# Kernel tuning notes

Hardware: AMD Instinct MI355X
Metric: run time of the kernel (lower is better)

The kernel has to match this reference:

```python
import jax, jax.numpy as jnp
import numpy as np

FP16_MIN = -65504.0
FP16_MAX = 65504.0

B, S, D, H = 2, 2048, 1024, 16
HD = D // H


def setup_inputs() -> dict:
    key = jax.random.key(0)
    ks = jax.random.split(key, 12)
    s = 0.02
    inp = {
        "x_q": jax.random.normal(ks[0], (B, S, D), jnp.float32),
        "x_k": jax.random.normal(ks[1], (B, S, D), jnp.float32),
        "x_v": jax.random.normal(ks[2], (B, S, D), jnp.float32),
        # causal mask [B, 1, S, S]; 0 entries are masked out
        "mask": jnp.broadcast_to(jnp.tril(jnp.ones((S, S), jnp.int32)), (B, 1, S, S)),
        "Wq": jax.random.normal(ks[3], (D, D), jnp.float32) * s,
        "bq": jnp.zeros((D,), jnp.float32),
        "Wk": jax.random.normal(ks[4], (D, D), jnp.float32) * s,
        "bk": jnp.zeros((D,), jnp.float32),
        "Wv": jax.random.normal(ks[5], (D, D), jnp.float32) * s,
        "bv": jnp.zeros((D,), jnp.float32),
        "Wo": jax.random.normal(ks[6], (D, D), jnp.float32) * s,
        "bo": jnp.zeros((D,), jnp.float32),
    }
    return inp


def _split_heads(x):
    # [B, S, D] -> [B, H, S, HD]
    b, s, _ = x.shape
    return x.reshape(b, s, H, HD).transpose(0, 2, 1, 3)


def reference(x_q, x_k, x_v, mask, Wq, bq, Wk, bk, Wv, bv, Wo, bo):
    scale = jnp.sqrt(jnp.float32(HD))
    q = _split_heads(x_q @ Wq + bq)  # [B,H,S,HD]
    k = _split_heads(x_k @ Wk + bk)
    v = _split_heads(x_v @ Wv + bv)

    scores = jnp.einsum("bhqd,bhkd->bhqk", q, k) / scale  # [B,H,S,S]
    scores = jnp.where(mask == 0, FP16_MIN, scores)
    scores = jnp.where(jnp.isneginf(scores), FP16_MIN, scores)
    scores = jnp.where(jnp.isposinf(scores), FP16_MAX, scores)

    probs = jax.nn.softmax(scores, axis=-1)  # dropout p=0.0 -> identity
    ctx = jnp.einsum("bhqk,bhkd->bhqd", probs, v)  # [B,H,S,HD]
    ctx = ctx.transpose(0, 2, 1, 3).reshape(x_q.shape[0], x_q.shape[1], D)
    out = ctx @ Wo + bo
    return out, probs
```

## Files before the change

### kernel.cpp

```cpp
#include <hip/hip_runtime.h>


typedef __bf16 bf16x8 __attribute__((ext_vector_type(8)));
typedef float f32x4 __attribute__((ext_vector_type(4)));

__device__ __forceinline__ unsigned short f2bf(float f) {
  unsigned int u = __builtin_bit_cast(unsigned int, f);
  u += 0x7fffu + ((u >> 16) & 1u);
  return (unsigned short)(u >> 16);
}
__device__ __forceinline__ float bf2f_lo(unsigned int u) {
  return __builtin_bit_cast(float, u << 16);
}
__device__ __forceinline__ float bf2f_hi(unsigned int u) {
  return __builtin_bit_cast(float, u & 0xffff0000u);
}

__global__ void transpose_w(const float* __restrict__ W0, const float* __restrict__ W1,
                            const float* __restrict__ W2, const float* __restrict__ W3,
                            unsigned short* __restrict__ Wt) {
  __shared__ float t[32][33];
  const int z = blockIdx.z;
  const float* W = (z == 0) ? W0 : (z == 1) ? W1 : (z == 2) ? W2 : W3;
  unsigned short* o = Wt + (size_t)z * 1048576u;
  const int n0 = blockIdx.x * 32, k0 = blockIdx.y * 32;
  const int tx = threadIdx.x, ty = threadIdx.y;
#pragma unroll
  for (int i = 0; i < 4; i++)
    t[ty + 8 * i][tx] = W[(size_t)(k0 + ty + 8 * i) * 1024 + n0 + tx];
  __syncthreads();
#pragma unroll
  for (int i = 0; i < 4; i++)
    o[(size_t)(n0 + ty + 8 * i) * 1024 + k0 + tx] = f2bf(t[tx][ty + 8 * i]);
}

__global__ __launch_bounds__(256) void gemm_kernel(
    const void* __restrict__ A0, const void* __restrict__ A1, const void* __restrict__ A2,
    const unsigned short* __restrict__ Wtb,
    const float* __restrict__ b0, const float* __restrict__ b1, const float* __restrict__ b2,
    void* __restrict__ O0, void* __restrict__ O1, void* __restrict__ O2,
    const int mode0) {
  __shared__ unsigned short Alds[64 * 72];
  const int z = blockIdx.z;
  const int mode = mode0 + z;
  const void* Av = (z == 0) ? A0 : (z == 1) ? A1 : A2;
  const float* bias = (z == 0) ? b0 : (z == 1) ? b1 : b2;
  void* outv = (z == 0) ? O0 : (z == 1) ? O1 : O2;
  const unsigned short* Wt = Wtb + (size_t)z * 1048576u;

  const int tid = threadIdx.x;
  const int lane = tid & 63;
  const int wave = tid >> 6;
  const int wm = wave >> 1, wn = wave & 1;
  const int m0 = blockIdx.y * 64, n0 = blockIdx.x * 128;
  const int g = lane >> 4, c = lane & 15;

  f32x4 acc[2][4];
#pragma unroll
  for (int i = 0; i < 2; i++)
#pragma unroll
    for (int j = 0; j < 4; j++) acc[i][j] = (f32x4){0.f, 0.f, 0.f, 0.f};

  const int srow = tid >> 2;
  const int sch = (tid & 3) * 16;

  uint4 pk0, pk1;
#define LOAD_PACK(KB)                                                             \
  if (mode < 3) {                                                                 \
    const float* A = (const float*)Av;                                            \
    const float4* src = (const float4*)(A + (size_t)(m0 + srow) * 1024 + (KB) + sch); \
    const float4 v0 = src[0], v1 = src[1], v2 = src[2], v3 = src[3];              \
    pk0.x = (unsigned int)f2bf(v0.x) | ((unsigned int)f2bf(v0.y) << 16);          \
    pk0.y = (unsigned int)f2bf(v0.z) | ((unsigned int)f2bf(v0.w) << 16);          \
    pk0.z = (unsigned int)f2bf(v1.x) | ((unsigned int)f2bf(v1.y) << 16);          \
    pk0.w = (unsigned int)f2bf(v1.z) | ((unsigned int)f2bf(v1.w) << 16);          \
    pk1.x = (unsigned int)f2bf(v2.x) | ((unsigned int)f2bf(v2.y) << 16);          \
    pk1.y = (unsigned int)f2bf(v2.z) | ((unsigned int)f2bf(v2.w) << 16);          \
    pk1.z = (unsigned int)f2bf(v3.x) | ((unsigned int)f2bf(v3.y) << 16);          \
    pk1.w = (unsigned int)f2bf(v3.z) | ((unsigned int)f2bf(v3.w) << 16);          \
  } else {                                                                        \
    const unsigned short* A = (const unsigned short*)Av;                          \
    const uint4* src = (const uint4*)(A + (size_t)(m0 + srow) * 1024 + (KB) + sch); \
    pk0 = src[0];                                                                 \
    pk1 = src[1];                                                                 \
  }

  LOAD_PACK(0);
  for (int kb = 0; kb < 1024; kb += 64) {
    *(uint4*)&Alds[srow * 72 + sch] = pk0;
    *(uint4*)&Alds[srow * 72 + sch + 8] = pk1;
    if (kb + 64 < 1024) { LOAD_PACK(kb + 64); }
    __syncthreads();

    bf16x8 af[2][2], bfr[4][2];
#pragma unroll
    for (int mi = 0; mi < 2; mi++)
#pragma unroll
      for (int kk = 0; kk < 2; kk++)
        af[mi][kk] = *(const bf16x8*)&Alds[(wm * 32 + mi * 16 + c) * 72 + kk * 32 + g * 8];
#pragma unroll
    for (int nf = 0; nf < 4; nf++)
#pragma unroll
      for (int kk = 0; kk < 2; kk++)
        bfr[nf][kk] = *(const bf16x8*)(Wt + (size_t)(n0 + wn * 64 + nf * 16 + c) * 1024 + kb + kk * 32 + g * 8);
#pragma unroll
    for (int kk = 0; kk < 2; kk++)
#pragma unroll
      for (int mi = 0; mi < 2; mi++)
#pragma unroll
        for (int nf = 0; nf < 4; nf++)
          acc[mi][nf] = __builtin_amdgcn_mfma_f32_16x16x32_bf16(af[mi][kk], bfr[nf][kk], acc[mi][nf], 0, 0, 0);
    __syncthreads();
  }
#undef LOAD_PACK

#pragma unroll
  for (int nf = 0; nf < 4; nf++) {
    const int col = n0 + wn * 64 + nf * 16 + c;
    const float bc = bias[col];
#pragma unroll
    for (int mi = 0; mi < 2; mi++) {
#pragma unroll
      for (int r = 0; r < 4; r++) {
        const int row = m0 + wm * 32 + mi * 16 + g * 4 + r;
        const float v = acc[mi][nf][r] + bc;
        if (mode == 0) {
          ((unsigned short*)outv)[(size_t)row * 1024 + col] = f2bf(v * 0.125f);
        } else if (mode == 1) {
          ((unsigned short*)outv)[(size_t)row * 1024 + col] = f2bf(v);
        } else if (mode == 2) {
          const int bb = row >> 11, s = row & 2047;
          ((unsigned short*)outv)[((size_t)(bb * 1024 + col)) * 2048 + s] = f2bf(v);
        } else {
          ((float*)outv)[(size_t)row * 1024 + col] = v;
        }
      }
    }
  }
}

__global__ __launch_bounds__(512, 4) void attn_kernel(
    const unsigned short* __restrict__ Q, const unsigned short* __restrict__ K,
    const unsigned short* __restrict__ Vt, float* __restrict__ probs,
    unsigned short* __restrict__ ctx) {
  __shared__ unsigned short Klds[64 * 72];
  __shared__ unsigned short Vlds[64 * 72];
  __shared__ unsigned short Plds[128 * 72];

  const int tid = threadIdx.x;
  const int lane = tid & 63, wave = tid >> 6;
  const int g = lane >> 4, c = lane & 15;
  const int bh = blockIdx.x;
  const int b = bh >> 4, h = bh & 15;
  const int q0 = blockIdx.y * 128;
  const int qrow0 = q0 + wave * 16;
  const int wave_kend = qrow0 + 16;

  const unsigned short* Qh = Q + ((size_t)(b * 2048 + qrow0)) * 1024 + h * 64;
  const unsigned short* Kh = K + ((size_t)b * 2048) * 1024 + h * 64;
  const unsigned short* Vh = Vt + ((size_t)bh) * 64 * 2048;
  float* Ph = probs + ((size_t)(bh * 2048 + q0)) * 2048;

  const bf16x8 qa0 = *(const bf16x8*)&Qh[(size_t)c * 1024 + g * 8];
  const bf16x8 qa1 = *(const bf16x8*)&Qh[(size_t)c * 1024 + 32 + g * 8];

  const int srow = tid >> 3;
  const int scol = (tid & 7) * 8;
  const int kb_end = q0 + 128;

  float lp[4] = {0.f, 0.f, 0.f, 0.f};
  f32x4 cacc[4];
#pragma unroll
  for (int nf = 0; nf < 4; nf++) cacc[nf] = (f32x4){0.f, 0.f, 0.f, 0.f};

  uint4 kreg = *(const uint4*)(Kh + (size_t)srow * 1024 + scol);
  uint4 vreg = *(const uint4*)(Vh + (size_t)srow * 2048 + scol);
  for (int kb = 0; kb < kb_end; kb += 64) {
    *(uint4*)&Klds[srow * 72 + scol] = kreg;
    *(uint4*)&Vlds[srow * 72 + scol] = vreg;
    if (kb + 64 < kb_end) {
      kreg = *(const uint4*)(Kh + (size_t)(kb + 64 + srow) * 1024 + scol);
      vreg = *(const uint4*)(Vh + (size_t)srow * 2048 + kb + 64 + scol);
    }
    __syncthreads();

    if (kb < wave_kend) {
      f32x4 sv[4];
#pragma unroll
      for (int sub = 0; sub < 4; sub++) {
        sv[sub] = (f32x4){0.f, 0.f, 0.f, 0.f};
        const unsigned short* Kr = &Klds[(sub * 16 + c) * 72];
        sv[sub] = __builtin_amdgcn_mfma_f32_16x16x32_bf16(qa0, *(const bf16x8*)&Kr[g * 8], sv[sub], 0, 0, 0);
        sv[sub] = __builtin_amdgcn_mfma_f32_16x16x32_bf16(qa1, *(const bf16x8*)&Kr[32 + g * 8], sv[sub], 0, 0, 0);
      }
      if (kb + 63 > qrow0) {
#pragma unroll
        for (int sub = 0; sub < 4; sub++)
#pragma unroll
          for (int r = 0; r < 4; r++)
            if (kb + sub * 16 + c > qrow0 + g * 4 + r) sv[sub][r] = -1e30f;
      }
#pragma unroll
      for (int sub = 0; sub < 4; sub++)
#pragma unroll
        for (int r = 0; r < 4; r++) {
          const float pu = __expf(sv[sub][r]);
          lp[r] += pu;
          Plds[(wave * 16 + g * 4 + r) * 72 + sub * 16 + c] = f2bf(pu);
        }
      const bf16x8 pa0 = *(const bf16x8*)&Plds[(wave * 16 + c) * 72 + g * 8];
      const bf16x8 pa1 = *(const bf16x8*)&Plds[(wave * 16 + c) * 72 + 32 + g * 8];
#pragma unroll
      for (int nf = 0; nf < 4; nf++) {
        const bf16x8 vf0 = *(const bf16x8*)&Vlds[(nf * 16 + c) * 72 + g * 8];
        const bf16x8 vf1 = *(const bf16x8*)&Vlds[(nf * 16 + c) * 72 + 32 + g * 8];
        cacc[nf] = __builtin_amdgcn_mfma_f32_16x16x32_bf16(pa0, vf0, cacc[nf], 0, 0, 0);
        cacc[nf] = __builtin_amdgcn_mfma_f32_16x16x32_bf16(pa1, vf1, cacc[nf], 0, 0, 0);
      }
    }
    __syncthreads();

    {
      const int prow = tid >> 2;
      const int pcb = (tid & 3) * 16;
      unsigned short* dst = (unsigned short*)Ph + (size_t)prow * 4096 + kb + pcb;
      const int rw_kend = q0 + (prow & ~15) + 16;
      if (kb < rw_kend) {
        *(uint4*)dst = *(const uint4*)&Plds[prow * 72 + pcb];
        *(uint4*)(dst + 8) = *(const uint4*)&Plds[prow * 72 + pcb + 8];
      } else {
        *(uint4*)dst = make_uint4(0u, 0u, 0u, 0u);
        *(uint4*)(dst + 8) = make_uint4(0u, 0u, 0u, 0u);
      }
    }
  }

#pragma unroll
  for (int off = 1; off < 16; off <<= 1)
#pragma unroll
    for (int r = 0; r < 4; r++) lp[r] += __shfl_xor(lp[r], off);
  float invl[4];
#pragma unroll
  for (int r = 0; r < 4; r++) invl[r] = 1.0f / lp[r];

#pragma unroll
  for (int nf = 0; nf < 4; nf++)
#pragma unroll
    for (int r = 0; r < 4; r++)
      ctx[((size_t)(b * 2048 + qrow0 + g * 4 + r)) * 1024 + h * 64 + nf * 16 + c] =
          f2bf(cacc[nf][r] * invl[r]);
}

__global__ __launch_bounds__(256) void norm_probs(float* __restrict__ probs) {
  __shared__ float wsum[4];
  const int rowIdx = blockIdx.x;
  const int q = rowIdx & 2047;
  const int kbe = ((q >> 7) + 1) << 7;
  float* base = probs + (size_t)rowIdx * 2048;
  const int t = threadIdx.x;
  const int c0 = t * 8;

  uint4 raw = make_uint4(0u, 0u, 0u, 0u);
  if (c0 < kbe) raw = *(const uint4*)((const unsigned short*)base + c0);
  float f0 = bf2f_lo(raw.x), f1 = bf2f_hi(raw.x), f2 = bf2f_lo(raw.y), f3 = bf2f_hi(raw.y);
  float f4 = bf2f_lo(raw.z), f5 = bf2f_hi(raw.z), f6 = bf2f_lo(raw.w), f7 = bf2f_hi(raw.w);

  float s = ((f0 + f1) + (f2 + f3)) + ((f4 + f5) + (f6 + f7));
#pragma unroll
  for (int off = 1; off < 64; off <<= 1) s += __shfl_xor(s, off);
  if ((t & 63) == 0) wsum[t >> 6] = s;
  __syncthreads();
  const float il = 1.0f / (wsum[0] + wsum[1] + wsum[2] + wsum[3]);

  float4* dst = (float4*)(base + c0);
  dst[0] = make_float4(f0 * il, f1 * il, f2 * il, f3 * il);
  dst[1] = make_float4(f4 * il, f5 * il, f6 * il, f7 * il);
}

extern "C" void kernel_launch(void* const* d_in, const int* in_sizes, int n_in,
                              void* d_out, int out_size, void* d_ws, size_t ws_size,
                              hipStream_t stream) {
  if (ws_size < (size_t)40 * 1024 * 1024) return;

  const float* xq = (const float*)d_in[0];
  const float* xk = (const float*)d_in[1];
  const float* xv = (const float*)d_in[2];
  const float* Wq = (const float*)d_in[4];
  const float* bq = (const float*)d_in[5];
  const float* Wk = (const float*)d_in[6];
  const float* bk = (const float*)d_in[7];
  const float* Wv = (const float*)d_in[8];
  const float* bv = (const float*)d_in[9];
  const float* Wo = (const float*)d_in[10];
  const float* bo = (const float*)d_in[11];

  unsigned short* ws = (unsigned short*)d_ws;
  unsigned short* Wt = ws;
  unsigned short* Qw = ws + (size_t)4 * 1048576u;
  unsigned short* Kw = Qw + 4194304u;
  unsigned short* Vtw = Kw + 4194304u;
  unsigned short* Cw = Vtw + 4194304u;

  float* out = (float*)d_out;
  float* probs = out + 4194304u;

  transpose_w<<<dim3(32, 32, 4), dim3(32, 8), 0, stream>>>(Wq, Wk, Wv, Wo, Wt);
  gemm_kernel<<<dim3(8, 64, 3), 256, 0, stream>>>(xq, xk, xv, Wt, bq, bk, bv,
                                                  Qw, Kw, Vtw, 0);
  attn_kernel<<<dim3(32, 16, 1), 512, 0, stream>>>(Qw, Kw, Vtw, probs, Cw);
  norm_probs<<<dim3(65536), 256, 0, stream>>>(probs);
  gemm_kernel<<<dim3(8, 64, 1), 256, 0, stream>>>(Cw, Cw, Cw, Wt + 3u * 1048576u,
                                                  bo, bo, bo, out, out, out, 3);
}
```

Measured before the change: 363.7 us.

## Double-buffer K/V tiles, reverse block order, per-wave P writes, wave-per-row normalize

```diff
diff --git a/kernel.cpp b/kernel.cpp
--- a/kernel.cpp
+++ b/kernel.cpp
@@ -143,8 +143,8 @@
     const unsigned short* __restrict__ Q, const unsigned short* __restrict__ K,
     const unsigned short* __restrict__ Vt, float* __restrict__ probs,
     unsigned short* __restrict__ ctx) {
-  __shared__ unsigned short Klds[64 * 72];
-  __shared__ unsigned short Vlds[64 * 72];
+  __shared__ unsigned short Klds[2][64 * 72];
+  __shared__ unsigned short Vlds[2][64 * 72];
   __shared__ unsigned short Plds[128 * 72];
 
   const int tid = threadIdx.x;
@@ -152,7 +152,7 @@
   const int g = lane >> 4, c = lane & 15;
   const int bh = blockIdx.x;
   const int b = bh >> 4, h = bh & 15;
-  const int q0 = blockIdx.y * 128;
+  const int q0 = (int)(gridDim.y - 1 - blockIdx.y) * 128;
   const int qrow0 = q0 + wave * 16;
   const int wave_kend = qrow0 + 16;
 
@@ -173,23 +173,38 @@
 #pragma unroll
   for (int nf = 0; nf < 4; nf++) cacc[nf] = (f32x4){0.f, 0.f, 0.f, 0.f};
 
-  uint4 kreg = *(const uint4*)(Kh + (size_t)srow * 1024 + scol);
-  uint4 vreg = *(const uint4*)(Vh + (size_t)srow * 2048 + scol);
-  for (int kb = 0; kb < kb_end; kb += 64) {
-    *(uint4*)&Klds[srow * 72 + scol] = kreg;
-    *(uint4*)&Vlds[srow * 72 + scol] = vreg;
-    if (kb + 64 < kb_end) {
-      kreg = *(const uint4*)(Kh + (size_t)(kb + 64 + srow) * 1024 + scol);
-      vreg = *(const uint4*)(Vh + (size_t)srow * 2048 + kb + 64 + scol);
+  const int prow = lane >> 2;
+  const int pcb = (lane & 3) * 16;
+  unsigned short* PwOut = (unsigned short*)Ph + (size_t)(wave * 16 + prow) * 4096 + pcb;
+  const unsigned short* PwLds = &Plds[(wave * 16 + prow) * 72 + pcb];
+
+  {
+    const uint4 k0 = *(const uint4*)(Kh + (size_t)srow * 1024 + scol);
+    const uint4 v0 = *(const uint4*)(Vh + (size_t)srow * 2048 + scol);
+    *(uint4*)&Klds[0][srow * 72 + scol] = k0;
+    *(uint4*)&Vlds[0][srow * 72 + scol] = v0;
+  }
+
+  int cur = 0;
+  for (int kb = 0; kb < kb_end; kb += 64, cur ^= 1) {
+    uint4 kn, vn;
+    const bool more = (kb + 64) < kb_end;
+    if (more) {
+      kn = *(const uint4*)(Kh + (size_t)(kb + 64 + srow) * 1024 + scol);
+      vn = *(const uint4*)(Vh + (size_t)srow * 2048 + kb + 64 + scol);
     }
     __syncthreads();
+    if (more) {
+      *(uint4*)&Klds[cur ^ 1][srow * 72 + scol] = kn;
+      *(uint4*)&Vlds[cur ^ 1][srow * 72 + scol] = vn;
+    }
 
     if (kb < wave_kend) {
       f32x4 sv[4];
 #pragma unroll
       for (int sub = 0; sub < 4; sub++) {
         sv[sub] = (f32x4){0.f, 0.f, 0.f, 0.f};
-        const unsigned short* Kr = &Klds[(sub * 16 + c) * 72];
+        const unsigned short* Kr = &Klds[cur][(sub * 16 + c) * 72];
         sv[sub] = __builtin_amdgcn_mfma_f32_16x16x32_bf16(qa0, *(const bf16x8*)&Kr[g * 8], sv[sub], 0, 0, 0);
         sv[sub] = __builtin_amdgcn_mfma_f32_16x16x32_bf16(qa1, *(const bf16x8*)&Kr[32 + g * 8], sv[sub], 0, 0, 0);
       }
@@ -212,26 +227,18 @@
       const bf16x8 pa1 = *(const bf16x8*)&Plds[(wave * 16 + c) * 72 + 32 + g * 8];
 #pragma unroll
       for (int nf = 0; nf < 4; nf++) {
-        const bf16x8 vf0 = *(const bf16x8*)&Vlds[(nf * 16 + c) * 72 + g * 8];
-        const bf16x8 vf1 = *(const bf16x8*)&Vlds[(nf * 16 + c) * 72 + 32 + g * 8];
+        const bf16x8 vf0 = *(const bf16x8*)&Vlds[cur][(nf * 16 + c) * 72 + g * 8];
+        const bf16x8 vf1 = *(const bf16x8*)&Vlds[cur][(nf * 16 + c) * 72 + 32 + g * 8];
         cacc[nf] = __builtin_amdgcn_mfma_f32_16x16x32_bf16(pa0, vf0, cacc[nf], 0, 0, 0);
         cacc[nf] = __builtin_amdgcn_mfma_f32_16x16x32_bf16(pa1, vf1, cacc[nf], 0, 0, 0);
       }
-    }
-    __syncthreads();
-
-    {
-      const int prow = tid >> 2;
-      const int pcb = (tid & 3) * 16;
-      unsigned short* dst = (unsigned short*)Ph + (size_t)prow * 4096 + kb + pcb;
-      const int rw_kend = q0 + (prow & ~15) + 16;
-      if (kb < rw_kend) {
-        *(uint4*)dst = *(const uint4*)&Plds[prow * 72 + pcb];
-        *(uint4*)(dst + 8) = *(const uint4*)&Plds[prow * 72 + pcb + 8];
-      } else {
-        *(uint4*)dst = make_uint4(0u, 0u, 0u, 0u);
-        *(uint4*)(dst + 8) = make_uint4(0u, 0u, 0u, 0u);
-      }
+      unsigned short* dst = PwOut + kb;
+      *(uint4*)dst = *(const uint4*)PwLds;
+      *(uint4*)(dst + 8) = *(const uint4*)(PwLds + 8);
+    } else {
+      unsigned short* dst = PwOut + kb;
+      *(uint4*)dst = make_uint4(0u, 0u, 0u, 0u);
+      *(uint4*)(dst + 8) = make_uint4(0u, 0u, 0u, 0u);
     }
   }
 
@@ -252,29 +259,39 @@
 }
 
 __global__ __launch_bounds__(256) void norm_probs(float* __restrict__ probs) {
-  __shared__ float wsum[4];
-  const int rowIdx = blockIdx.x;
-  const int q = rowIdx & 2047;
-  const int kbe = ((q >> 7) + 1) << 7;
-  float* base = probs + (size_t)rowIdx * 2048;
-  const int t = threadIdx.x;
-  const int c0 = t * 8;
-
-  uint4 raw = make_uint4(0u, 0u, 0u, 0u);
-  if (c0 < kbe) raw = *(const uint4*)((const unsigned short*)base + c0);
-  float f0 = bf2f_lo(raw.x), f1 = bf2f_hi(raw.x), f2 = bf2f_lo(raw.y), f3 = bf2f_hi(raw.y);
-  float f4 = bf2f_lo(raw.z), f5 = bf2f_hi(raw.z), f6 = bf2f_lo(raw.w), f7 = bf2f_hi(raw.w);
-
-  float s = ((f0 + f1) + (f2 + f3)) + ((f4 + f5) + (f6 + f7));
-#pragma unroll
-  for (int off = 1; off < 64; off <<= 1) s += __shfl_xor(s, off);
-  if ((t & 63) == 0) wsum[t >> 6] = s;
-  __syncthreads();
-  const float il = 1.0f / (wsum[0] + wsum[1] + wsum[2] + wsum[3]);
-
-  float4* dst = (float4*)(base + c0);
-  dst[0] = make_float4(f0 * il, f1 * il, f2 * il, f3 * il);
-  dst[1] = make_float4(f4 * il, f5 * il, f6 * il, f7 * il);
+  const int wv = (blockIdx.x * 256 + threadIdx.x) >> 6;
+  const int lane = threadIdx.x & 63;
+  for (int row = wv; row < 65536; row += 8192) {
+    const int q = row & 2047;
+    const int kbe = ((q >> 7) + 1) << 7;
+    float* base = probs + (size_t)row * 2048;
+    const int c0 = lane * 32;
+    uint4 r0 = make_uint4(0u, 0u, 0u, 0u), r1 = r0, r2 = r0, r3 = r0;
+    if (c0 < kbe) {
+      const uint4* src = (const uint4*)((const unsigned short*)base + c0);
+      r0 = src[0]; r1 = src[1]; r2 = src[2]; r3 = src[3];
+    }
+    float f[32];
+#pragma unroll
+    for (int i = 0; i < 4; i++) {
+      const uint4 rr = (i == 0) ? r0 : (i == 1) ? r1 : (i == 2) ? r2 : r3;
+      f[i * 8 + 0] = bf2f_lo(rr.x); f[i * 8 + 1] = bf2f_hi(rr.x);
+      f[i * 8 + 2] = bf2f_lo(rr.y); f[i * 8 + 3] = bf2f_hi(rr.y);
+      f[i * 8 + 4] = bf2f_lo(rr.z); f[i * 8 + 5] = bf2f_hi(rr.z);
+      f[i * 8 + 6] = bf2f_lo(rr.w); f[i * 8 + 7] = bf2f_hi(rr.w);
+    }
+    float s = 0.f;
+#pragma unroll
+    for (int i = 0; i < 32; i++) s += f[i];
+#pragma unroll
+    for (int off = 1; off < 64; off <<= 1) s += __shfl_xor(s, off);
+    const float il = 1.0f / s;
+    float4* dst = (float4*)(base + c0);
+#pragma unroll
+    for (int i = 0; i < 8; i++)
+      dst[i] = make_float4(f[i * 4 + 0] * il, f[i * 4 + 1] * il,
+                           f[i * 4 + 2] * il, f[i * 4 + 3] * il);
+  }
 }
 
 extern "C" void kernel_launch(void* const* d_in, const int* in_sizes, int n_in,
@@ -308,7 +325,7 @@
   gemm_kernel<<<dim3(8, 64, 3), 256, 0, stream>>>(xq, xk, xv, Wt, bq, bk, bv,
                                                   Qw, Kw, Vtw, 0);
   attn_kernel<<<dim3(32, 16, 1), 512, 0, stream>>>(Qw, Kw, Vtw, probs, Cw);
-  norm_probs<<<dim3(65536), 256, 0, stream>>>(probs);
+  norm_probs<<<dim3(2048), 256, 0, stream>>>(probs);
   gemm_kernel<<<dim3(8, 64, 1), 256, 0, stream>>>(Cw, Cw, Cw, Wt + 3u * 1048576u,
                                                   bo, bo, bo, out, out, out, 3);
 }
```

Result: slower. 499.0 us (+37.2%).

## Double-buffer K/V in attention, fold log2e into Q scale, reverse block order

Applied to the files above, without the earlier changes.

```diff
diff --git a/kernel.cpp b/kernel.cpp
--- a/kernel.cpp
+++ b/kernel.cpp
@@ -8,6 +8,9 @@
   unsigned int u = __builtin_bit_cast(unsigned int, f);
   u += 0x7fffu + ((u >> 16) & 1u);
   return (unsigned short)(u >> 16);
+}
+__device__ __forceinline__ unsigned short f2bf_hw(float f) {
+  return __builtin_bit_cast(unsigned short, (__bf16)f);
 }
 __device__ __forceinline__ float bf2f_lo(unsigned int u) {
   return __builtin_bit_cast(float, u << 16);
@@ -125,7 +128,7 @@
         const int row = m0 + wm * 32 + mi * 16 + g * 4 + r;
         const float v = acc[mi][nf][r] + bc;
         if (mode == 0) {
-          ((unsigned short*)outv)[(size_t)row * 1024 + col] = f2bf(v * 0.125f);
+          ((unsigned short*)outv)[(size_t)row * 1024 + col] = f2bf(v * 0.1803368801111244f);
         } else if (mode == 1) {
           ((unsigned short*)outv)[(size_t)row * 1024 + col] = f2bf(v);
         } else if (mode == 2) {
@@ -143,8 +146,8 @@
     const unsigned short* __restrict__ Q, const unsigned short* __restrict__ K,
     const unsigned short* __restrict__ Vt, float* __restrict__ probs,
     unsigned short* __restrict__ ctx) {
-  __shared__ unsigned short Klds[64 * 72];
-  __shared__ unsigned short Vlds[64 * 72];
+  __shared__ unsigned short Klds[2][64 * 72];
+  __shared__ unsigned short Vlds[2][64 * 72];
   __shared__ unsigned short Plds[128 * 72];
 
   const int tid = threadIdx.x;
@@ -152,7 +155,7 @@
   const int g = lane >> 4, c = lane & 15;
   const int bh = blockIdx.x;
   const int b = bh >> 4, h = bh & 15;
-  const int q0 = blockIdx.y * 128;
+  const int q0 = (int)(gridDim.y - 1 - blockIdx.y) * 128;
   const int qrow0 = q0 + wave * 16;
   const int wave_kend = qrow0 + 16;
 
@@ -173,23 +176,36 @@
 #pragma unroll
   for (int nf = 0; nf < 4; nf++) cacc[nf] = (f32x4){0.f, 0.f, 0.f, 0.f};
 
-  uint4 kreg = *(const uint4*)(Kh + (size_t)srow * 1024 + scol);
-  uint4 vreg = *(const uint4*)(Vh + (size_t)srow * 2048 + scol);
-  for (int kb = 0; kb < kb_end; kb += 64) {
-    *(uint4*)&Klds[srow * 72 + scol] = kreg;
-    *(uint4*)&Vlds[srow * 72 + scol] = vreg;
-    if (kb + 64 < kb_end) {
-      kreg = *(const uint4*)(Kh + (size_t)(kb + 64 + srow) * 1024 + scol);
-      vreg = *(const uint4*)(Vh + (size_t)srow * 2048 + kb + 64 + scol);
+  const int prow = lane >> 2;
+  const int pcb = (lane & 3) * 16;
+  unsigned short* PwOut = (unsigned short*)Ph + (size_t)(wave * 16 + prow) * 4096 + pcb;
+  const unsigned short* PwLds = &Plds[(wave * 16 + prow) * 72 + pcb];
+
+  {
+    *(uint4*)&Klds[0][srow * 72 + scol] = *(const uint4*)(Kh + (size_t)srow * 1024 + scol);
+    *(uint4*)&Vlds[0][srow * 72 + scol] = *(const uint4*)(Vh + (size_t)srow * 2048 + scol);
+  }
+
+  int cur = 0;
+  for (int kb = 0; kb < kb_end; kb += 64, cur ^= 1) {
+    uint4 kn, vn;
+    const bool more = (kb + 64) < kb_end;
+    if (more) {
+      kn = *(const uint4*)(Kh + (size_t)(kb + 64 + srow) * 1024 + scol);
+      vn = *(const uint4*)(Vh + (size_t)srow * 2048 + kb + 64 + scol);
     }
     __syncthreads();
+    if (more) {
+      *(uint4*)&Klds[cur ^ 1][srow * 72 + scol] = kn;
+      *(uint4*)&Vlds[cur ^ 1][srow * 72 + scol] = vn;
+    }
 
     if (kb < wave_kend) {
       f32x4 sv[4];
 #pragma unroll
       for (int sub = 0; sub < 4; sub++) {
         sv[sub] = (f32x4){0.f, 0.f, 0.f, 0.f};
-        const unsigned short* Kr = &Klds[(sub * 16 + c) * 72];
+        const unsigned short* Kr = &Klds[cur][(sub * 16 + c) * 72];
         sv[sub] = __builtin_amdgcn_mfma_f32_16x16x32_bf16(qa0, *(const bf16x8*)&Kr[g * 8], sv[sub], 0, 0, 0);
         sv[sub] = __builtin_amdgcn_mfma_f32_16x16x32_bf16(qa1, *(const bf16x8*)&Kr[32 + g * 8], sv[sub], 0, 0, 0);
       }
@@ -204,34 +220,26 @@
       for (int sub = 0; sub < 4; sub++)
 #pragma unroll
         for (int r = 0; r < 4; r++) {
-          const float pu = __expf(sv[sub][r]);
+          const float pu = __builtin_amdgcn_exp2f(sv[sub][r]);
           lp[r] += pu;
-          Plds[(wave * 16 + g * 4 + r) * 72 + sub * 16 + c] = f2bf(pu);
+          Plds[(wave * 16 + g * 4 + r) * 72 + sub * 16 + c] = f2bf_hw(pu);
         }
       const bf16x8 pa0 = *(const bf16x8*)&Plds[(wave * 16 + c) * 72 + g * 8];
       const bf16x8 pa1 = *(const bf16x8*)&Plds[(wave * 16 + c) * 72 + 32 + g * 8];
 #pragma unroll
       for (int nf = 0; nf < 4; nf++) {
-        const bf16x8 vf0 = *(const bf16x8*)&Vlds[(nf * 16 + c) * 72 + g * 8];
-        const bf16x8 vf1 = *(const bf16x8*)&Vlds[(nf * 16 + c) * 72 + 32 + g * 8];
+        const bf16x8 vf0 = *(const bf16x8*)&Vlds[cur][(nf * 16 + c) * 72 + g * 8];
+        const bf16x8 vf1 = *(const bf16x8*)&Vlds[cur][(nf * 16 + c) * 72 + 32 + g * 8];
         cacc[nf] = __builtin_amdgcn_mfma_f32_16x16x32_bf16(pa0, vf0, cacc[nf], 0, 0, 0);
         cacc[nf] = __builtin_amdgcn_mfma_f32_16x16x32_bf16(pa1, vf1, cacc[nf], 0, 0, 0);
       }
-    }
-    __syncthreads();
-
-    {
-      const int prow = tid >> 2;
-      const int pcb = (tid & 3) * 16;
-      unsigned short* dst = (unsigned short*)Ph + (size_t)prow * 4096 + kb + pcb;
-      const int rw_kend = q0 + (prow & ~15) + 16;
-      if (kb < rw_kend) {
-        *(uint4*)dst = *(const uint4*)&Plds[prow * 72 + pcb];
-        *(uint4*)(dst + 8) = *(const uint4*)&Plds[prow * 72 + pcb + 8];
-      } else {
-        *(uint4*)dst = make_uint4(0u, 0u, 0u, 0u);
-        *(uint4*)(dst + 8) = make_uint4(0u, 0u, 0u, 0u);
-      }
+      unsigned short* dst = PwOut + kb;
+      *(uint4*)dst = *(const uint4*)PwLds;
+      *(uint4*)(dst + 8) = *(const uint4*)(PwLds + 8);
+    } else {
+      unsigned short* dst = PwOut + kb;
+      *(uint4*)dst = make_uint4(0u, 0u, 0u, 0u);
+      *(uint4*)(dst + 8) = make_uint4(0u, 0u, 0u, 0u);
     }
   }
 
@@ -248,7 +256,7 @@
 #pragma unroll
     for (int r = 0; r < 4; r++)
       ctx[((size_t)(b * 2048 + qrow0 + g * 4 + r)) * 1024 + h * 64 + nf * 16 + c] =
-          f2bf(cacc[nf][r] * invl[r]);
+          f2bf_hw(cacc[nf][r] * invl[r]);
 }
 
 __global__ __launch_bounds__(256) void norm_probs(float* __restrict__ probs) {
```

Measured after the change: 353.6 us. 2.8% less time.
